# Kernel tuning notes

Hardware: AMD Instinct MI355X
Metric: run time of the kernel (lower is better)

Reference implementation:

```python
import jax, jax.numpy as jnp
import numpy as np

THRESH = 0.3
DECAY = 0.5


def spike_fn(x):
    # Heaviside threshold (forward only)
    return (x > THRESH).astype(x.dtype)


def setup_inputs() -> dict:
    key = jax.random.key(0)
    k_in, k0, k1, k2 = jax.random.split(key, 4)
    B, D0, T = 128, 512, 512
    inputs = jax.random.uniform(k_in, (B, D0, T), dtype=jnp.float32)
    w0 = jax.random.normal(k0, (512, 1024), dtype=jnp.float32)
    w1 = jax.random.normal(k1, (1024, 1024), dtype=jnp.float32)
    w2 = jax.random.normal(k2, (1024, 512), dtype=jnp.float32)
    return {"inputs": inputs, "w0": w0, "w1": w1, "w2": w2}


def reference(inputs, w0, w1, w2):
    ws = (w0, w1, w2)
    B = inputs.shape[0]
    layer_dims = tuple(w.shape[1] for w in ws)

    # time-major: [T, B, D0]
    xs = jnp.transpose(inputs, (2, 0, 1))

    mem0 = tuple(jnp.zeros((B, d), dtype=inputs.dtype) for d in layer_dims)
    spk0 = tuple(jnp.zeros((B, d), dtype=inputs.dtype) for d in layer_dims)

    def step(carry, x_t):
        mems, spikes = carry
        prev_spike = x_t  # layer-0 spikes come straight from the input
        new_mems, new_spikes = [], []
        for i, w in enumerate(ws):
            # leaky integrate with reset-by-spike, then fire
            mem = mems[i] * DECAY * (1.0 - spikes[i]) + prev_spike @ w
            s = spike_fn(mem)
            new_mems.append(mem)
            new_spikes.append(s)
            prev_spike = s
        return (tuple(new_mems), tuple(new_spikes)), None

    (_, spikes_final), _ = jax.lax.scan(step, (mem0, spk0), xs)
    return spikes_final[-1]
```

## Files before the change

### kernel.cpp

```cpp
#include <hip/hip_runtime.h>


typedef __bf16 bf16;
typedef __attribute__((ext_vector_type(8))) __bf16 bf16x8;
typedef __attribute__((ext_vector_type(16))) float f32x16;
typedef unsigned long long u64;

#define B_   128
#define D0_  512
#define T_   512
#define TS_  128
#define N1_  1024
#define N2_  1024
#define N3_  512
#define MFMA32(a,b,c) __builtin_amdgcn_mfma_f32_32x32x16_bf16((a),(b),(c),0,0,0)

#define GL2LDS(g, l) __builtin_amdgcn_global_load_lds( \
    (const __attribute__((address_space(1))) void*)(g), \
    (__attribute__((address_space(3))) void*)(l), 16, 0, 0)

#define WAIT_BARRIER() do { \
    asm volatile("s_waitcnt vmcnt(0)" ::: "memory"); \
    __builtin_amdgcn_s_barrier(); } while (0)

#define VM8() asm volatile("s_waitcnt vmcnt(8)" ::: "memory")
#define VM0() asm volatile("s_waitcnt vmcnt(0)" ::: "memory")


__global__ __launch_bounds__(256)
void split_w(const float* __restrict__ W, bf16* __restrict__ WTh, bf16* __restrict__ WTl,
             int K, int N)
{
    __shared__ float tile[32][33];
    const int k0 = blockIdx.x * 32, n0 = blockIdx.y * 32;
    const int tx = threadIdx.x & 31, ty = threadIdx.x >> 5;
#pragma unroll
    for (int r = 0; r < 4; ++r)
        tile[ty + r * 8][tx] = W[(size_t)(k0 + ty + r * 8) * N + n0 + tx];
    __syncthreads();
#pragma unroll
    for (int r = 0; r < 4; ++r) {
        int nl = ty + r * 8;
        float v = tile[tx][nl];
        bf16 h = (bf16)v;
        size_t o = (size_t)(n0 + nl) * K + k0 + tx;
        WTh[o] = h;
        WTl[o] = (bf16)(v - (float)h);
    }
}

__global__ __launch_bounds__(256)
void split_x(const float* __restrict__ in, bf16* __restrict__ Xh, bf16* __restrict__ Xl)
{
    __shared__ float tile[32][33];
    const int b = blockIdx.z, d0 = blockIdx.x * 32, t0 = blockIdx.y * 32;
    const int tx = threadIdx.x & 31, ty = threadIdx.x >> 5;
#pragma unroll
    for (int r = 0; r < 4; ++r)
        tile[ty + r * 8][tx] = in[((size_t)b * D0_ + d0 + ty + r * 8) * T_ + t0 + tx];
    __syncthreads();
    const int s = t0 >> 7;
#pragma unroll
    for (int r = 0; r < 4; ++r) {
        int t  = t0 + ty + r * 8;
        int tl = t & (TS_ - 1);
        float v = tile[tx][ty + r * 8];
        bf16 h = (bf16)v;
        size_t o = (((size_t)s * B_ + b) * TS_ + tl) * D0_ + d0 + tx;
        Xh[o] = h;
        Xl[o] = (bf16)(v - (float)h);
    }
}

__device__ __forceinline__ bf16x8 expand8(unsigned v)
{
    union { unsigned u[4]; bf16x8 h; } r;
    const unsigned p = v * 0x8001u;
#pragma unroll
    for (int i = 0; i < 4; ++i)
        r.u[i] = ((p >> (2 * i)) & 0x10001u) * 0x3F80u;
    return r.h;
}

__global__ __launch_bounds__(256, 2)
void snn_layer0(const bf16* __restrict__ Ah, const bf16* __restrict__ Al,
                const bf16* __restrict__ WTh, const bf16* __restrict__ WTl,
                u64* __restrict__ bitsOut)
{
    constexpr int K = D0_;
    __shared__ char smem[65536];
    bf16* sA0  = (bf16*)(smem);
    bf16* sAl0 = (bf16*)(smem + 8192);
    bf16* sB0  = (bf16*)(smem + 16384);
    bf16* sBl0 = (bf16*)(smem + 24576);
    bf16* sA1  = (bf16*)(smem + 32768);
    bf16* sAl1 = (bf16*)(smem + 40960);
    bf16* sB1  = (bf16*)(smem + 49152);
    bf16* sBl1 = (bf16*)(smem + 57344);
    float* If  = (float*)smem;

    const int tid = threadIdx.x, lane = tid & 63, w = tid >> 6;
    const int wm = w & 1, wn = w >> 1;
    const int l31 = lane & 31, kh = lane >> 5;
    const int bid = blockIdx.x;
    const int b  = (bid & 7) | ((bid >> 6) << 3);
    const int nb = ((bid >> 3) & 7) * 128;

    const int i4 = lane >> 2, c4 = lane & 3;
    const int csrc = c4 ^ ((i4 >> 1) & 3);
    const bf16* gBh = WTh + (size_t)(nb + w * 32 + i4) * K + csrc * 8;
    const bf16* gBl = WTl + (size_t)(nb + w * 32 + i4) * K + csrc * 8;
    const int wT = w * 32 * 32;

    int rA[2], rB[2], swA[2], swB[2];
#pragma unroll
    for (int i = 0; i < 2; ++i) {
        rA[i] = wm * 64 + i * 32 + l31;
        rB[i] = wn * 64 + i * 32 + l31;
        swA[i] = (rA[i] >> 1) & 3;
        swB[i] = (rB[i] >> 1) & 3;
    }

    float cm = 0.f, cs = 0.f;
    const int scol = tid & 63;
    float* Ifb = If + (tid >> 6) * 4096;

#define STAGE0(dA, dAl, dBh, dBl, go)                                          \
    do {                                                                       \
        _Pragma("unroll")                                                      \
        for (int inst = 0; inst < 2; ++inst) {                                 \
            GL2LDS(gA  + (size_t)(inst * 16) * K + (go), (dA)  + wT + inst * 16 * 32); \
            GL2LDS(gAl + (size_t)(inst * 16) * K + (go), (dAl) + wT + inst * 16 * 32); \
            GL2LDS(gBh + (size_t)(inst * 16) * K + (go), (dBh) + wT + inst * 16 * 32); \
            GL2LDS(gBl + (size_t)(inst * 16) * K + (go), (dBl) + wT + inst * 16 * 32); \
        }                                                                      \
    } while (0)

#define KSTEP0(cA, cAl, cBh, cBl)                                              \
    do {                                                                       \
        bf16x8 a[2][2], al2[2][2];                                             \
        _Pragma("unroll")                                                      \
        for (int mi = 0; mi < 2; ++mi)                                         \
            _Pragma("unroll")                                                  \
            for (int h = 0; h < 2; ++h) {                                      \
                const int off = rA[mi] * 32 + (((2 * h + kh) ^ swA[mi]) * 8);  \
                a[mi][h]   = *(const bf16x8*)((cA) + off);                     \
                al2[mi][h] = *(const bf16x8*)((cAl) + off);                    \
            }                                                                  \
        _Pragma("unroll")                                                      \
        for (int h = 0; h < 2; ++h) {                                          \
            bf16x8 bh[2], bl[2];                                               \
            _Pragma("unroll")                                                  \
            for (int ni = 0; ni < 2; ++ni) {                                   \
                const int off = rB[ni] * 32 + (((2 * h + kh) ^ swB[ni]) * 8);  \
                bh[ni] = *(const bf16x8*)((cBh) + off);                        \
                bl[ni] = *(const bf16x8*)((cBl) + off);                        \
            }                                                                  \
            _Pragma("unroll")                                                  \
            for (int ni = 0; ni < 2; ++ni)                                     \
                _Pragma("unroll")                                              \
                for (int mi = 0; mi < 2; ++mi)                                 \
                    acc[mi][ni] = MFMA32(a[mi][h], bh[ni], acc[mi][ni]);       \
            _Pragma("unroll")                                                  \
            for (int ni = 0; ni < 2; ++ni)                                     \
                _Pragma("unroll")                                              \
                for (int mi = 0; mi < 2; ++mi)                                 \
                    acc[mi][ni] = MFMA32(al2[mi][h], bh[ni], acc[mi][ni]);     \
            _Pragma("unroll")                                                  \
            for (int ni = 0; ni < 2; ++ni)                                     \
                _Pragma("unroll")                                              \
                for (int mi = 0; mi < 2; ++mi)                                 \
                    acc[mi][ni] = MFMA32(a[mi][h], bl[ni], acc[mi][ni]);       \
        }                                                                      \
        WAIT_BARRIER();                                                        \
    } while (0)

#pragma unroll 1
    for (int s = 0; s < T_ / TS_; ++s) {
        const size_t arow = ((size_t)s * B_ + b) * TS_;
        const bf16* gA  = Ah + (arow + w * 32 + i4) * K + csrc * 8;
        const bf16* gAl = Al + (arow + w * 32 + i4) * K + csrc * 8;

        STAGE0(sA0, sAl0, sB0, sBl0, 0);
        WAIT_BARRIER();

        f32x16 acc[2][2] = {};

#pragma unroll 1
        for (int ks = 0; ks < K / 32; ks += 2) {
            STAGE0(sA1, sAl1, sB1, sBl1, (ks + 1) * 32);
            KSTEP0(sA0, sAl0, sB0, sBl0);
            if (ks + 2 < K / 32)
                STAGE0(sA0, sAl0, sB0, sBl0, (ks + 2) * 32);
            KSTEP0(sA1, sAl1, sB1, sBl1);
        }

        u64 word0 = 0, word1 = 0;
        if (wm == 0) {
#pragma unroll
            for (int ni = 0; ni < 2; ++ni)
#pragma unroll
                for (int mi = 0; mi < 2; ++mi)
#pragma unroll
                    for (int r = 0; r < 16; ++r) {
                        const int tt = mi * 32 + (r & 3) + 8 * (r >> 2) + 4 * kh;
                        If[wn * 4096 + tt * 64 + ni * 32 + l31] = acc[mi][ni][r];
                    }
        }
        __syncthreads();
        if (tid < 128) {
            float m = cm, sp = cs;
#pragma unroll 4
            for (int tt = 0; tt < 64; ++tt) {
                m = m * 0.5f * (1.0f - sp) + Ifb[tt * 64 + scol];
                const bool fire = m > 0.3f;
                sp = fire ? 1.0f : 0.0f;
                u64 bal = __ballot(fire);
                if ((tid & 63) == tt) word0 = bal;
            }
            cm = m; cs = sp;
        }
        __syncthreads();
        if (wm == 1) {
#pragma unroll
            for (int ni = 0; ni < 2; ++ni)
#pragma unroll
                for (int mi = 0; mi < 2; ++mi)
#pragma unroll
                    for (int r = 0; r < 16; ++r) {
                        const int tt = mi * 32 + (r & 3) + 8 * (r >> 2) + 4 * kh;
                        If[wn * 4096 + tt * 64 + ni * 32 + l31] = acc[mi][ni][r];
                    }
        }
        __syncthreads();
        if (tid < 128) {
            float m = cm, sp = cs;
#pragma unroll 4
            for (int tt = 0; tt < 64; ++tt) {
                m = m * 0.5f * (1.0f - sp) + Ifb[tt * 64 + scol];
                const bool fire = m > 0.3f;
                sp = fire ? 1.0f : 0.0f;
                u64 bal = __ballot(fire);
                if ((tid & 63) == tt) word1 = bal;
            }
            cm = m; cs = sp;
            u64* dst = bitsOut + ((size_t)s * B_ + b) * 2048;
            const int j8 = (nb >> 6) + (tid >> 6);
            const int t0 = tid & 63, t1 = 64 + (tid & 63);
            dst[t0 * 16 + (j8 ^ (t0 & 15))] = word0;
            dst[t1 * 16 + (j8 ^ (t1 & 15))] = word1;
        }
        __syncthreads();
    }
#undef STAGE0
#undef KSTEP0
}

template<bool WRITE_BITS>
__global__ __launch_bounds__(256, 2)
void snn_layer_bits(const u64* __restrict__ bitsIn,
                    const bf16* __restrict__ WTh, const bf16* __restrict__ WTl,
                    u64* __restrict__ bitsOut, float* __restrict__ outp, int N)
{
    constexpr int K = 1024;
    __shared__ char smem[81920];
    char* bitsLds = smem;
    float* If = (float*)(smem + 16384);

    const int tid = threadIdx.x, lane = tid & 63, w = tid >> 6;
    const int wm = w & 1, wn = w >> 1;
    const int l31 = lane & 31, kh = lane >> 5;
    const int b = blockIdx.y;
    const int nb = blockIdx.x * 128;

    bf16* wbase = (bf16*)(smem + 16384 + w * 16384);

    const int i4 = lane >> 2, c4 = lane & 3;
    const int csrc = c4 ^ ((i4 >> 1) & 3);
    const bf16* gBh = WTh + (size_t)(nb + wn * 64 + i4) * K + csrc * 8;
    const bf16* gBl = WTl + (size_t)(nb + wn * 64 + i4) * K + csrc * 8;

    const int sw3 = (l31 >> 1) & 3;
    const int sh8 = 8 * kh;
    const int rA0 = wm * 64 + l31, rA1 = wm * 64 + 32 + l31;
    const int rA0b = rA0 * 128, rA1b = rA1 * 128;
    const int s15 = l31 & 15;

    float cm = 0.f, cs = 0.f;

#define STAGEP(j, go)                                                          \
    do {                                                                       \
        _Pragma("unroll")                                                      \
        for (int inst = 0; inst < 4; ++inst) {                                 \
            GL2LDS(gBh + (size_t)(inst * 16) * K + (go), wbase + (j) * 4096 + inst * 512); \
            GL2LDS(gBl + (size_t)(inst * 16) * K + (go), wbase + (j) * 4096 + 2048 + inst * 512); \
        }                                                                      \
    } while (0)

#define KSTEPP(j, x0, x1)                                                      \
    do {                                                                       \
        const bf16* cBh = wbase + (j) * 4096;                                  \
        const bf16* cBl = cBh + 2048;                                          \
        _Pragma("unroll")                                                      \
        for (int h = 0; h < 2; ++h) {                                          \
            bf16x8 a0 = expand8(((x0) >> (16 * h + sh8)) & 0xFFu);             \
            bf16x8 a1 = expand8(((x1) >> (16 * h + sh8)) & 0xFFu);             \
            bf16x8 bh[2], bl[2];                                               \
            _Pragma("unroll")                                                  \
            for (int ni = 0; ni < 2; ++ni) {                                   \
                const int off = (ni * 32 + l31) * 32 + (((2 * h + kh) ^ sw3) * 8); \
                bh[ni] = *(const bf16x8*)(cBh + off);                          \
                bl[ni] = *(const bf16x8*)(cBl + off);                          \
            }                                                                  \
            __builtin_amdgcn_s_setprio(1);                                     \
            acc[0][0] = MFMA32(a0, bh[0], acc[0][0]);                          \
            acc[1][0] = MFMA32(a1, bh[0], acc[1][0]);                          \
            acc[0][1] = MFMA32(a0, bh[1], acc[0][1]);                          \
            acc[1][1] = MFMA32(a1, bh[1], acc[1][1]);                          \
            acc[0][0] = MFMA32(a0, bl[0], acc[0][0]);                          \
            acc[1][0] = MFMA32(a1, bl[0], acc[1][0]);                          \
            acc[0][1] = MFMA32(a0, bl[1], acc[0][1]);                          \
            acc[1][1] = MFMA32(a1, bl[1], acc[1][1]);                          \
            __builtin_amdgcn_s_setprio(0);                                     \
        }                                                                      \
    } while (0)

#pragma unroll 1
    for (int s = 0; s < T_ / TS_; ++s) {
        {
            const char* src = (const char*)bitsIn + ((size_t)s * B_ + b) * 16384;
#pragma unroll
            for (int i = 0; i < 4; ++i)
                GL2LDS(src + (w * 4 + i) * 1024 + lane * 16,
                       bitsLds + (w * 4 + i) * 1024);
        }
        WAIT_BARRIER();
        STAGEP(0, 0);

        f32x16 acc[2][2] = {};

#pragma unroll 1
        for (int ks = 0; ks < 30; ks += 2) {
            const int pi = ks >> 1;
            const u64 wa0 = *(const u64*)(bitsLds + rA0b + ((pi ^ s15) << 3));
            const u64 wa1 = *(const u64*)(bitsLds + rA1b + ((pi ^ s15) << 3));
            STAGEP(1, (ks + 1) * 32);
            VM8();
            KSTEPP(0, (unsigned)wa0, (unsigned)wa1);
            STAGEP(0, (ks + 2) * 32);
            VM8();
            KSTEPP(1, (unsigned)(wa0 >> 32), (unsigned)(wa1 >> 32));
        }
        {
            const u64 wa0 = *(const u64*)(bitsLds + rA0b + ((15 ^ s15) << 3));
            const u64 wa1 = *(const u64*)(bitsLds + rA1b + ((15 ^ s15) << 3));
            STAGEP(1, 31 * 32);
            VM8();
            KSTEPP(0, (unsigned)wa0, (unsigned)wa1);
            VM0();
            KSTEPP(1, (unsigned)(wa0 >> 32), (unsigned)(wa1 >> 32));
        }

        __syncthreads();
#pragma unroll
        for (int ni = 0; ni < 2; ++ni)
#pragma unroll
            for (int mi = 0; mi < 2; ++mi)
#pragma unroll
                for (int r = 0; r < 16; ++r) {
                    const int tt = wm * 64 + mi * 32 + (r & 3) + 8 * (r >> 2) + 4 * kh;
                    If[tt * 128 + wn * 64 + ni * 32 + l31] = acc[mi][ni][r];
                }
        __syncthreads();
        u64 word0 = 0, word1 = 0;
        if (tid < 128) {
            float m = cm, sp = cs;
#pragma unroll 4
            for (int tt = 0; tt < 128; ++tt) {
                m = m * 0.5f * (1.0f - sp) + If[tt * 128 + tid];
                const bool fire = m > 0.3f;
                sp = fire ? 1.0f : 0.0f;
                if constexpr (WRITE_BITS) {
                    u64 bal = __ballot(fire);
                    if ((tid & 63) == (tt & 63)) {
                        if (tt < 64) word0 = bal; else word1 = bal;
                    }
                }
            }
            cm = m; cs = sp;
            if constexpr (WRITE_BITS) {
                u64* dst = bitsOut + ((size_t)s * B_ + b) * 2048;
                const int j8 = (nb >> 6) + (tid >> 6);
                const int t0 = tid & 63, t1 = 64 + (tid & 63);
                dst[t0 * 16 + (j8 ^ (t0 & 15))] = word0;
                dst[t1 * 16 + (j8 ^ (t1 & 15))] = word1;
            } else {
                if (s == T_ / TS_ - 1)
                    outp[(size_t)b * N + nb + tid] = cs;
            }
        }
        __syncthreads();
    }
#undef STAGEP
#undef KSTEPP
}

extern "C" void kernel_launch(void* const* d_in, const int* in_sizes, int n_in,
                              void* d_out, int out_size, void* d_ws, size_t ws_size,
                              hipStream_t stream)
{
    const float* x  = (const float*)d_in[0];
    const float* w0 = (const float*)d_in[1];
    const float* w1 = (const float*)d_in[2];
    const float* w2 = (const float*)d_in[3];
    float* out = (float*)d_out;

    char* p = (char*)d_ws;
    bf16* w0h = (bf16*)p;  p += (size_t)N1_ * D0_ * 2;
    bf16* w0l = (bf16*)p;  p += (size_t)N1_ * D0_ * 2;
    bf16* w1h = (bf16*)p;  p += (size_t)N2_ * N1_ * 2;
    bf16* w1l = (bf16*)p;  p += (size_t)N2_ * N1_ * 2;
    bf16* w2h = (bf16*)p;  p += (size_t)N3_ * N2_ * 2;
    bf16* w2l = (bf16*)p;  p += (size_t)N3_ * N2_ * 2;
    bf16* Xh  = (bf16*)p;  p += (size_t)T_ * B_ * D0_ * 2;
    bf16* Xl  = (bf16*)p;  p += (size_t)T_ * B_ * D0_ * 2;
    u64* bits0 = (u64*)p;  p += (size_t)(T_/TS_) * B_ * TS_ * (N1_/8);
    u64* bits1 = (u64*)p;  p += (size_t)(T_/TS_) * B_ * TS_ * (N2_/8);

    split_w<<<dim3(D0_/32, N1_/32), 256, 0, stream>>>(w0, w0h, w0l, D0_, N1_);
    split_w<<<dim3(N1_/32, N2_/32), 256, 0, stream>>>(w1, w1h, w1l, N1_, N2_);
    split_w<<<dim3(N2_/32, N3_/32), 256, 0, stream>>>(w2, w2h, w2l, N2_, N3_);
    split_x<<<dim3(D0_/32, T_/32, B_), 256, 0, stream>>>(x, Xh, Xl);

    snn_layer0<<<dim3(B_ * (N1_/128)), 256, 0, stream>>>(Xh, Xl, w0h, w0l, bits0);
    snn_layer_bits<true ><<<dim3(N2_/128, B_), 256, 0, stream>>>(
        bits0, w1h, w1l, bits1, nullptr, N2_);
    snn_layer_bits<false><<<dim3(N3_/128, B_), 256, 0, stream>>>(
        bits1, w2h, w2l, nullptr, out, N3_);
}
```

Baseline: 874.9 us.

## Pre-swizzle layer weights into MFMA fragment order and load directly to registers

Adds a weight-split kernel that writes W1/W2 hi/lo bf16 halves in per-lane MFMA B-fragment order. The bit-input layers then load weight fragments straight from global memory into registers with a one-step software prefetch, instead of staging through LDS with global_load_lds and waitcnt. Each wave now covers 32 output columns across all 128 timesteps (4 M-tiles) rather than a 2x2 split, and the trailing barrier is dropped. This removes LDS traffic and waits for weights but relies on L2/L1 caching of fragments shared across the 128 batch blocks, and raises register pressure.

```diff
diff --git a/kernel.cpp b/kernel.cpp
--- a/kernel.cpp
+++ b/kernel.cpp
@@ -23,9 +23,6 @@
     asm volatile("s_waitcnt vmcnt(0)" ::: "memory"); \
     __builtin_amdgcn_s_barrier(); } while (0)
 
-#define VM8() asm volatile("s_waitcnt vmcnt(8)" ::: "memory")
-#define VM0() asm volatile("s_waitcnt vmcnt(0)" ::: "memory")
-
 
 __global__ __launch_bounds__(256)
 void split_w(const float* __restrict__ W, bf16* __restrict__ WTh, bf16* __restrict__ WTl,
@@ -46,6 +43,25 @@
         size_t o = (size_t)(n0 + nl) * K + k0 + tx;
         WTh[o] = h;
         WTl[o] = (bf16)(v - (float)h);
+    }
+}
+
+__global__ __launch_bounds__(64)
+void split_wf(const float* __restrict__ W, bf16* __restrict__ Fh, bf16* __restrict__ Fl,
+              int K, int N)
+{
+    const int l = threadIdx.x;
+    const int kc = blockIdx.x;
+    const int np = blockIdx.y;
+    const int c  = np * 32 + (l & 31);
+    const int k0 = kc * 16 + (l >> 5) * 8;
+    const size_t ob = (((size_t)np * (K / 16) + kc) * 64 + l) * 8;
+#pragma unroll
+    for (int e = 0; e < 8; ++e) {
+        float v = W[(size_t)(k0 + e) * N + c];
+        bf16 h = (bf16)v;
+        Fh[ob + e] = h;
+        Fl[ob + e] = (bf16)(v - (float)h);
     }
 }
 
@@ -259,69 +275,53 @@
 template<bool WRITE_BITS>
 __global__ __launch_bounds__(256, 2)
 void snn_layer_bits(const u64* __restrict__ bitsIn,
-                    const bf16* __restrict__ WTh, const bf16* __restrict__ WTl,
+                    const bf16* __restrict__ WFh, const bf16* __restrict__ WFl,
                     u64* __restrict__ bitsOut, float* __restrict__ outp, int N)
 {
-    constexpr int K = 1024;
+    constexpr int K = 1024, KC = K / 16;
     __shared__ char smem[81920];
     char* bitsLds = smem;
     float* If = (float*)(smem + 16384);
 
     const int tid = threadIdx.x, lane = tid & 63, w = tid >> 6;
-    const int wm = w & 1, wn = w >> 1;
     const int l31 = lane & 31, kh = lane >> 5;
     const int b = blockIdx.y;
     const int nb = blockIdx.x * 128;
 
-    bf16* wbase = (bf16*)(smem + 16384 + w * 16384);
-
-    const int i4 = lane >> 2, c4 = lane & 3;
-    const int csrc = c4 ^ ((i4 >> 1) & 3);
-    const bf16* gBh = WTh + (size_t)(nb + wn * 64 + i4) * K + csrc * 8;
-    const bf16* gBl = WTl + (size_t)(nb + wn * 64 + i4) * K + csrc * 8;
-
-    const int sw3 = (l31 >> 1) & 3;
+    const bf16* wfh = WFh + ((size_t)((nb >> 5) + w) * KC) * 512 + lane * 8;
+    const bf16* wfl = WFl + ((size_t)((nb >> 5) + w) * KC) * 512 + lane * 8;
+
     const int sh8 = 8 * kh;
-    const int rA0 = wm * 64 + l31, rA1 = wm * 64 + 32 + l31;
-    const int rA0b = rA0 * 128, rA1b = rA1 * 128;
     const int s15 = l31 & 15;
+    int rbase[4];
+#pragma unroll
+    for (int mi = 0; mi < 4; ++mi)
+        rbase[mi] = (mi * 32 + l31) * 128;
 
     float cm = 0.f, cs = 0.f;
 
-#define STAGEP(j, go)                                                          \
+#define CPAIR(cb0, cb1, cb2, cb3)                                              \
     do {                                                                       \
         _Pragma("unroll")                                                      \
-        for (int inst = 0; inst < 4; ++inst) {                                 \
-            GL2LDS(gBh + (size_t)(inst * 16) * K + (go), wbase + (j) * 4096 + inst * 512); \
-            GL2LDS(gBl + (size_t)(inst * 16) * K + (go), wbase + (j) * 4096 + 2048 + inst * 512); \
-        }                                                                      \
-    } while (0)
-
-#define KSTEPP(j, x0, x1)                                                      \
-    do {                                                                       \
-        const bf16* cBh = wbase + (j) * 4096;                                  \
-        const bf16* cBl = cBh + 2048;                                          \
-        _Pragma("unroll")                                                      \
-        for (int h = 0; h < 2; ++h) {                                          \
-            bf16x8 a0 = expand8(((x0) >> (16 * h + sh8)) & 0xFFu);             \
-            bf16x8 a1 = expand8(((x1) >> (16 * h + sh8)) & 0xFFu);             \
-            bf16x8 bh[2], bl[2];                                               \
-            _Pragma("unroll")                                                  \
-            for (int ni = 0; ni < 2; ++ni) {                                   \
-                const int off = (ni * 32 + l31) * 32 + (((2 * h + kh) ^ sw3) * 8); \
-                bh[ni] = *(const bf16x8*)(cBh + off);                          \
-                bl[ni] = *(const bf16x8*)(cBl + off);                          \
+        for (int st = 0; st < 2; ++st) {                                       \
+            _Pragma("unroll")                                                  \
+            for (int h = 0; h < 2; ++h) {                                      \
+                const int j = st * 2 + h;                                      \
+                bf16x8 a0 = expand8((unsigned)((cb0) >> (32 * st + 16 * h + sh8)) & 0xFFu); \
+                bf16x8 a1 = expand8((unsigned)((cb1) >> (32 * st + 16 * h + sh8)) & 0xFFu); \
+                bf16x8 a2 = expand8((unsigned)((cb2) >> (32 * st + 16 * h + sh8)) & 0xFFu); \
+                bf16x8 a3 = expand8((unsigned)((cb3) >> (32 * st + 16 * h + sh8)) & 0xFFu); \
+                __builtin_amdgcn_s_setprio(1);                                 \
+                acc[0] = MFMA32(a0, ch[j], acc[0]);                            \
+                acc[1] = MFMA32(a1, ch[j], acc[1]);                            \
+                acc[2] = MFMA32(a2, ch[j], acc[2]);                            \
+                acc[3] = MFMA32(a3, ch[j], acc[3]);                            \
+                acc[0] = MFMA32(a0, cl[j], acc[0]);                            \
+                acc[1] = MFMA32(a1, cl[j], acc[1]);                            \
+                acc[2] = MFMA32(a2, cl[j], acc[2]);                            \
+                acc[3] = MFMA32(a3, cl[j], acc[3]);                            \
+                __builtin_amdgcn_s_setprio(0);                                 \
             }                                                                  \
-            __builtin_amdgcn_s_setprio(1);                                     \
-            acc[0][0] = MFMA32(a0, bh[0], acc[0][0]);                          \
-            acc[1][0] = MFMA32(a1, bh[0], acc[1][0]);                          \
-            acc[0][1] = MFMA32(a0, bh[1], acc[0][1]);                          \
-            acc[1][1] = MFMA32(a1, bh[1], acc[1][1]);                          \
-            acc[0][0] = MFMA32(a0, bl[0], acc[0][0]);                          \
-            acc[1][0] = MFMA32(a1, bl[0], acc[1][0]);                          \
-            acc[0][1] = MFMA32(a0, bl[1], acc[0][1]);                          \
-            acc[1][1] = MFMA32(a1, bl[1], acc[1][1]);                          \
-            __builtin_amdgcn_s_setprio(0);                                     \
         }                                                                      \
     } while (0)
 
@@ -335,42 +335,48 @@
                        bitsLds + (w * 4 + i) * 1024);
         }
         WAIT_BARRIER();
-        STAGEP(0, 0);
-
-        f32x16 acc[2][2] = {};
+
+        f32x16 acc[4] = {};
+
+        u64 cb0, cb1, cb2, cb3;
+        bf16x8 ch[4], cl[4];
+        cb0 = *(const u64*)(bitsLds + rbase[0] + ((0 ^ s15) << 3));
+        cb1 = *(const u64*)(bitsLds + rbase[1] + ((0 ^ s15) << 3));
+        cb2 = *(const u64*)(bitsLds + rbase[2] + ((0 ^ s15) << 3));
+        cb3 = *(const u64*)(bitsLds + rbase[3] + ((0 ^ s15) << 3));
+#pragma unroll
+        for (int j = 0; j < 4; ++j) {
+            ch[j] = *(const bf16x8*)(wfh + (size_t)j * 512);
+            cl[j] = *(const bf16x8*)(wfl + (size_t)j * 512);
+        }
 
 #pragma unroll 1
-        for (int ks = 0; ks < 30; ks += 2) {
-            const int pi = ks >> 1;
-            const u64 wa0 = *(const u64*)(bitsLds + rA0b + ((pi ^ s15) << 3));
-            const u64 wa1 = *(const u64*)(bitsLds + rA1b + ((pi ^ s15) << 3));
-            STAGEP(1, (ks + 1) * 32);
-            VM8();
-            KSTEPP(0, (unsigned)wa0, (unsigned)wa1);
-            STAGEP(0, (ks + 2) * 32);
-            VM8();
-            KSTEPP(1, (unsigned)(wa0 >> 32), (unsigned)(wa1 >> 32));
-        }
-        {
-            const u64 wa0 = *(const u64*)(bitsLds + rA0b + ((15 ^ s15) << 3));
-            const u64 wa1 = *(const u64*)(bitsLds + rA1b + ((15 ^ s15) << 3));
-            STAGEP(1, 31 * 32);
-            VM8();
-            KSTEPP(0, (unsigned)wa0, (unsigned)wa1);
-            VM0();
-            KSTEPP(1, (unsigned)(wa0 >> 32), (unsigned)(wa1 >> 32));
-        }
-
-        __syncthreads();
-#pragma unroll
-        for (int ni = 0; ni < 2; ++ni)
-#pragma unroll
-            for (int mi = 0; mi < 2; ++mi)
-#pragma unroll
-                for (int r = 0; r < 16; ++r) {
-                    const int tt = wm * 64 + mi * 32 + (r & 3) + 8 * (r >> 2) + 4 * kh;
-                    If[tt * 128 + wn * 64 + ni * 32 + l31] = acc[mi][ni][r];
-                }
+        for (int pi = 0; pi < 15; ++pi) {
+            u64 nb0, nb1, nb2, nb3;
+            bf16x8 nh[4], nl[4];
+            nb0 = *(const u64*)(bitsLds + rbase[0] + (((pi + 1) ^ s15) << 3));
+            nb1 = *(const u64*)(bitsLds + rbase[1] + (((pi + 1) ^ s15) << 3));
+            nb2 = *(const u64*)(bitsLds + rbase[2] + (((pi + 1) ^ s15) << 3));
+            nb3 = *(const u64*)(bitsLds + rbase[3] + (((pi + 1) ^ s15) << 3));
+#pragma unroll
+            for (int j = 0; j < 4; ++j) {
+                nh[j] = *(const bf16x8*)(wfh + (size_t)((pi + 1) * 4 + j) * 512);
+                nl[j] = *(const bf16x8*)(wfl + (size_t)((pi + 1) * 4 + j) * 512);
+            }
+            CPAIR(cb0, cb1, cb2, cb3);
+            cb0 = nb0; cb1 = nb1; cb2 = nb2; cb3 = nb3;
+#pragma unroll
+            for (int j = 0; j < 4; ++j) { ch[j] = nh[j]; cl[j] = nl[j]; }
+        }
+        CPAIR(cb0, cb1, cb2, cb3);
+
+#pragma unroll
+        for (int mi = 0; mi < 4; ++mi)
+#pragma unroll
+            for (int r = 0; r < 16; ++r) {
+                const int tt = mi * 32 + (r & 3) + 8 * (r >> 2) + 4 * kh;
+                If[tt * 128 + w * 32 + l31] = acc[mi][r];
+            }
         __syncthreads();
         u64 word0 = 0, word1 = 0;
         if (tid < 128) {
@@ -399,10 +405,8 @@
                     outp[(size_t)b * N + nb + tid] = cs;
             }
         }
-        __syncthreads();
-    }
-#undef STAGEP
-#undef KSTEPP
+    }
+#undef CPAIR
 }
 
 extern "C" void kernel_launch(void* const* d_in, const int* in_sizes, int n_in,
@@ -416,25 +420,25 @@
     float* out = (float*)d_out;
 
     char* p = (char*)d_ws;
-    bf16* w0h = (bf16*)p;  p += (size_t)N1_ * D0_ * 2;
-    bf16* w0l = (bf16*)p;  p += (size_t)N1_ * D0_ * 2;
-    bf16* w1h = (bf16*)p;  p += (size_t)N2_ * N1_ * 2;
-    bf16* w1l = (bf16*)p;  p += (size_t)N2_ * N1_ * 2;
-    bf16* w2h = (bf16*)p;  p += (size_t)N3_ * N2_ * 2;
-    bf16* w2l = (bf16*)p;  p += (size_t)N3_ * N2_ * 2;
-    bf16* Xh  = (bf16*)p;  p += (size_t)T_ * B_ * D0_ * 2;
-    bf16* Xl  = (bf16*)p;  p += (size_t)T_ * B_ * D0_ * 2;
+    bf16* w0h  = (bf16*)p; p += (size_t)N1_ * D0_ * 2;
+    bf16* w0l  = (bf16*)p; p += (size_t)N1_ * D0_ * 2;
+    bf16* wf1h = (bf16*)p; p += (size_t)N2_ * N1_ * 2;
+    bf16* wf1l = (bf16*)p; p += (size_t)N2_ * N1_ * 2;
+    bf16* wf2h = (bf16*)p; p += (size_t)N3_ * N2_ * 2;
+    bf16* wf2l = (bf16*)p; p += (size_t)N3_ * N2_ * 2;
+    bf16* Xh   = (bf16*)p; p += (size_t)T_ * B_ * D0_ * 2;
+    bf16* Xl   = (bf16*)p; p += (size_t)T_ * B_ * D0_ * 2;
     u64* bits0 = (u64*)p;  p += (size_t)(T_/TS_) * B_ * TS_ * (N1_/8);
     u64* bits1 = (u64*)p;  p += (size_t)(T_/TS_) * B_ * TS_ * (N2_/8);
 
     split_w<<<dim3(D0_/32, N1_/32), 256, 0, stream>>>(w0, w0h, w0l, D0_, N1_);
-    split_w<<<dim3(N1_/32, N2_/32), 256, 0, stream>>>(w1, w1h, w1l, N1_, N2_);
-    split_w<<<dim3(N2_/32, N3_/32), 256, 0, stream>>>(w2, w2h, w2l, N2_, N3_);
+    split_wf<<<dim3(N1_/16, N2_/32), 64, 0, stream>>>(w1, wf1h, wf1l, N1_, N2_);
+    split_wf<<<dim3(N2_/16, N3_/32), 64, 0, stream>>>(w2, wf2h, wf2l, N2_, N3_);
     split_x<<<dim3(D0_/32, T_/32, B_), 256, 0, stream>>>(x, Xh, Xl);
 
     snn_layer0<<<dim3(B_ * (N1_/128)), 256, 0, stream>>>(Xh, Xl, w0h, w0l, bits0);
     snn_layer_bits<true ><<<dim3(N2_/128, B_), 256, 0, stream>>>(
-        bits0, w1h, w1l, bits1, nullptr, N2_);
+        bits0, wf1h, wf1l, bits1, nullptr, N2_);
     snn_layer_bits<false><<<dim3(N3_/128, B_), 256, 0, stream>>>(
-        bits1, w2h, w2l, nullptr, out, N3_);
-}
+        bits1, wf2h, wf2l, nullptr, out, N3_);
+}
```

New measurement: 831.9 us. -4.9%, faster.
